# Optimization experiments

Measured on AMD Instinct MI355X. Metric: run time of the kernel, lower is better.

Reference implementation:

```python
import jax, jax.numpy as jnp
import numpy as np

VOCAB, S, D, H, DH, L, W1S, DFF = 50265, 4096, 768, 12, 64, 2, 256, 3072


def layer_norm(x, g, b, eps=1e-5):
    m = jnp.mean(x, axis=-1, keepdims=True)
    v = jnp.mean((x - m) ** 2, axis=-1, keepdims=True)
    return (x - m) * jax.lax.rsqrt(v + eps) * g + b


def sliding_global_attn(q, k, v, att, w=W1S):
    # q,k,v: [B,H,S,Dh]; att: [B,S] float (1 real / 0 pad). Longformer-style
    # sliding window (one-sided w) + global attention on token 0.
    B, nh, S_, Dh = q.shape
    nc = S_ // w
    q = q * (Dh ** -0.5)
    k_pad = jnp.pad(k, ((0, 0), (0, 0), (w, w), (0, 0)))
    v_pad = jnp.pad(v, ((0, 0), (0, 0), (w, w), (0, 0)))
    idx = jnp.arange(nc)[:, None] * w + jnp.arange(3 * w)[None, :]  # [nc,3w] into padded axis
    k_band = k_pad[:, :, idx]  # [B,H,nc,3w,Dh]
    v_band = v_pad[:, :, idx]
    qc = q.reshape(B, nh, nc, w, Dh)
    s_loc = jnp.einsum('bhcqd,bhckd->bhcqk', qc, k_band)  # [B,H,nc,w,3w]
    rel = jnp.arange(3 * w)[None, :] - jnp.arange(w)[:, None]  # [w,3w]
    band_ok = (rel >= 0) & (rel <= 2 * w)
    key_abs = idx - w  # [nc,3w] absolute key positions
    in_seq = (key_abs >= 0) & (key_abs < S_) & (key_abs != 0)  # token 0 handled by global column
    key_real = att[:, jnp.clip(key_abs, 0, S_ - 1)] > 0  # [B,nc,3w]
    valid = band_ok[None, None, None] & in_seq[None, None, :, None, :] & key_real[:, None, :, None, :]
    s_loc = jnp.where(valid, s_loc, -1e9)
    s_g = jnp.einsum('bhcqd,bhd->bhcq', qc, k[:, :, 0])  # global key column
    p = jax.nn.softmax(jnp.concatenate([s_g[..., None], s_loc], axis=-1), axis=-1)
    out = (jnp.einsum('bhcq,bhd->bhcqd', p[..., 0], v[:, :, 0])
           + jnp.einsum('bhcqk,bhckd->bhcqd', p[..., 1:], v_band)).reshape(B, nh, S_, Dh)
    # global token 0 attends to everything
    s0 = jnp.where(att[:, None, :] > 0, jnp.einsum('bhd,bhsd->bhs', q[:, :, 0], k), -1e9)
    out0 = jnp.einsum('bhs,bhsd->bhd', jax.nn.softmax(s0, axis=-1), v)
    return out.at[:, :, 0].set(out0)


def setup_inputs() -> dict:
    key = jax.random.key(0)
    ks = jax.random.split(key, 16)
    sc = 0.02
    inp = {
        'input_ids': jax.random.randint(ks[0], (2, S), 0, VOCAB, dtype=jnp.int64)
        if jax.config.jax_enable_x64 else jax.random.randint(ks[0], (2, S), 0, VOCAB, dtype=jnp.int32),
        'attention_mask': jnp.ones((2, S), dtype=jnp.int32),
        'word_emb': sc * jax.random.normal(ks[1], (VOCAB, D), jnp.float32),
        'pos_emb': sc * jax.random.normal(ks[2], (S, D), jnp.float32),
        'emb_ln_g': jnp.ones((D,), jnp.float32), 'emb_ln_b': jnp.zeros((D,), jnp.float32),
        'Wq': sc * jax.random.normal(ks[3], (L, D, D), jnp.float32), 'bq': jnp.zeros((L, D), jnp.float32),
        'Wk': sc * jax.random.normal(ks[4], (L, D, D), jnp.float32), 'bk': jnp.zeros((L, D), jnp.float32),
        'Wv': sc * jax.random.normal(ks[5], (L, D, D), jnp.float32), 'bv': jnp.zeros((L, D), jnp.float32),
        'Wo': sc * jax.random.normal(ks[6], (L, D, D), jnp.float32), 'bo': jnp.zeros((L, D), jnp.float32),
        'ln1_g': jnp.ones((L, D), jnp.float32), 'ln1_b': jnp.zeros((L, D), jnp.float32),
        'Wf1': sc * jax.random.normal(ks[7], (L, D, DFF), jnp.float32), 'bf1': jnp.zeros((L, DFF), jnp.float32),
        'Wf2': sc * jax.random.normal(ks[8], (L, DFF, D), jnp.float32), 'bf2': jnp.zeros((L, D), jnp.float32),
        'ln2_g': jnp.ones((L, D), jnp.float32), 'ln2_b': jnp.zeros((L, D), jnp.float32),
        'Wh1': sc * jax.random.normal(ks[9], (D, 256), jnp.float32), 'bh1': jnp.zeros((256,), jnp.float32),
        'Wh2': sc * jax.random.normal(ks[10], (256, 14), jnp.float32), 'bh2': jnp.zeros((14,), jnp.float32),
    }
    return inp


def reference(input_ids, attention_mask, word_emb, pos_emb, emb_ln_g, emb_ln_b,
              Wq, bq, Wk, bk, Wv, bv, Wo, bo, ln1_g, ln1_b,
              Wf1, bf1, Wf2, bf2, ln2_g, ln2_b, Wh1, bh1, Wh2, bh2):
    B, S_ = input_ids.shape
    att = attention_mask.astype(jnp.float32)
    x = word_emb[input_ids] + pos_emb[None, :S_, :]
    x = layer_norm(x, emb_ln_g, emb_ln_b)
    for l in range(L):
        def heads(w, b):
            return (x @ w + b).reshape(B, S_, H, DH).transpose(0, 2, 1, 3)
        q = heads(Wq[l], bq[l]); k = heads(Wk[l], bk[l]); v = heads(Wv[l], bv[l])
        a = sliding_global_attn(q, k, v, att)
        a = a.transpose(0, 2, 1, 3).reshape(B, S_, D) @ Wo[l] + bo[l]
        x = layer_norm(x + a, ln1_g[l], ln1_b[l])
        f = jax.nn.gelu(x @ Wf1[l] + bf1[l]) @ Wf2[l] + bf2[l]
        x = layer_norm(x + f, ln2_g[l], ln2_b[l])
    # masked mean pool
    m = att[..., None]
    pooled = jnp.sum(x * m, axis=1) / jnp.clip(jnp.sum(m, axis=1), 1e-9)
    h = jax.nn.relu(pooled @ Wh1 + bh1)
    return jax.nn.sigmoid(h @ Wh2 + bh2) * 4.0
```

## Files before the change

### kernel.cpp

```cpp
#include <hip/hip_runtime.h>
#include <hip/hip_bf16.h>
#include <math.h>

#define S_LEN 4096
#define D_MODEL 768
#define NHEAD 12
#define DH 64
#define NLAYER 2
#define DFF 3072
#define BATCH 2
#define QSTR 2304

typedef __attribute__((ext_vector_type(8))) __bf16 bf16x8;
typedef __attribute__((ext_vector_type(4))) float f32x4;
typedef __attribute__((ext_vector_type(16))) float f32x16;

__device__ __forceinline__ unsigned short f2bf_bits(float f) {
  unsigned int u = __float_as_uint(f);
  unsigned int r = (u + 0x7fffu + ((u >> 16) & 1u)) >> 16;
  return (unsigned short)r;
}

__device__ __forceinline__ float bf2f(unsigned short u) {
  return __uint_as_float(((unsigned int)u) << 16);
}

__device__ __forceinline__ unsigned int cvtpk_bf16(float lo, float hi) {
  unsigned int d;
  asm("v_cvt_pk_bf16_f32 %0, %1, %2" : "=v"(d) : "v"(lo), "v"(hi));
  return d;
}

__device__ __forceinline__ float gelu_fast(float x) {
  float u = 0.7978845608028654f * (x + 0.044715f * x * x * x);
  float t2 = fminf(fmaxf(2.f * u, -18.f), 18.f);
  float e = __expf(t2);
  return 0.5f * x * (1.f + (e - 1.f) / (e + 1.f));
}

#define ASYNC_COPY16(gsrc, ldst)                                       \
  __builtin_amdgcn_global_load_lds(                                    \
      (const __attribute__((address_space(1))) void*)(gsrc),           \
      (__attribute__((address_space(3))) void*)(ldst), 16, 0, 0)

#define MFMA_BF16(a, b, c) __builtin_amdgcn_mfma_f32_16x16x32_bf16(a, b, c, 0, 0, 0)
#define MFMA32_BF16(a, b, c) __builtin_amdgcn_mfma_f32_32x32x16_bf16(a, b, c, 0, 0, 0)

__device__ __forceinline__ float blk_sum256(float v, float* lds) {
#pragma unroll
  for (int off = 32; off > 0; off >>= 1) v += __shfl_down(v, off, 64);
  __syncthreads();
  if ((threadIdx.x & 63) == 0) lds[threadIdx.x >> 6] = v;
  __syncthreads();
  return lds[0] + lds[1] + lds[2] + lds[3];
}

__global__ __launch_bounds__(256) void wconv_kernel(
    const float* __restrict__ Wq, const float* __restrict__ Wk,
    const float* __restrict__ Wv, const float* __restrict__ Wo,
    const float* __restrict__ Wf1, const float* __restrict__ Wf2,
    unsigned short* __restrict__ Wbf) {
  int id = blockIdx.x;
  const float* src;
  unsigned short* dst;
  int K, N, t;
  if (id < 4608) {
    int m = id / 576;
    t = id % 576;
    int layer = m >> 2, which = m & 3;
    const float* s = (which == 0) ? Wq : (which == 1) ? Wk : (which == 2) ? Wv : Wo;
    src = s + (size_t)layer * 589824;
    dst = Wbf + (size_t)layer * 7077888 + (size_t)which * 589824;
    K = 768; N = 768;
  } else if (id < 9216) {
    int j = id - 4608;
    int layer = j / 2304;
    t = j % 2304;
    src = Wf1 + (size_t)layer * 2359296;
    dst = Wbf + (size_t)layer * 7077888 + 2359296;
    K = 768; N = 3072;
  } else {
    int j = id - 9216;
    int layer = j / 2304;
    t = j % 2304;
    src = Wf2 + (size_t)layer * 2359296;
    dst = Wbf + (size_t)layer * 7077888 + 4718592;
    K = 3072; N = 768;
  }
  int tiles_n = N >> 5;
  int tk = t / tiles_n, tn = t % tiles_n;
  __shared__ float tile[32][33];
  int c = threadIdx.x & 31, r0 = threadIdx.x >> 5;
#pragma unroll
  for (int p = 0; p < 4; ++p) {
    int r = r0 + p * 8;
    tile[r][c] = src[(size_t)(tk * 32 + r) * N + tn * 32 + c];
  }
  __syncthreads();
#pragma unroll
  for (int p = 0; p < 4; ++p) {
    int r = r0 + p * 8;
    dst[(size_t)(tn * 32 + r) * K + tk * 32 + c] = f2bf_bits(tile[c][r]);
  }
}

__global__ __launch_bounds__(256) void embed_ln_kernel(
    const int* __restrict__ ids, const float* __restrict__ wemb,
    const float* __restrict__ pemb, const float* __restrict__ g,
    const float* __restrict__ b, unsigned short* __restrict__ Xb) {
  int row = blockIdx.x;
  int s = row % S_LEN;
  int id = ids[row];
  const float* we = wemb + (size_t)id * D_MODEL;
  const float* pe = pemb + (size_t)s * D_MODEL;
  int t = threadIdx.x;
  __shared__ float lds[4];
  float v0 = we[t] + pe[t];
  float v1 = we[t + 256] + pe[t + 256];
  float v2 = we[t + 512] + pe[t + 512];
  float mean = blk_sum256(v0 + v1 + v2, lds) * (1.f / 768.f);
  float d0 = v0 - mean, d1 = v1 - mean, d2 = v2 - mean;
  float var = blk_sum256(d0 * d0 + d1 * d1 + d2 * d2, lds) * (1.f / 768.f);
  float rs = rsqrtf(var + 1e-5f);
  unsigned short* xb = Xb + (size_t)row * D_MODEL;
  xb[t]       = f2bf_bits(d0 * rs * g[t] + b[t]);
  xb[t + 256] = f2bf_bits(d1 * rs * g[t + 256] + b[t + 256]);
  xb[t + 512] = f2bf_bits(d2 * rs * g[t + 512] + b[t + 512]);
}

__global__ __launch_bounds__(256) void ln_kernel(
    const float* __restrict__ T, const float* __restrict__ g,
    const float* __restrict__ b, unsigned short* __restrict__ Xb) {
  int row = blockIdx.x;
  const float* tp = T + (size_t)row * D_MODEL;
  int t = threadIdx.x;
  __shared__ float lds[4];
  float v0 = tp[t], v1 = tp[t + 256], v2 = tp[t + 512];
  float mean = blk_sum256(v0 + v1 + v2, lds) * (1.f / 768.f);
  float d0 = v0 - mean, d1 = v1 - mean, d2 = v2 - mean;
  float var = blk_sum256(d0 * d0 + d1 * d1 + d2 * d2, lds) * (1.f / 768.f);
  float rs = rsqrtf(var + 1e-5f);
  unsigned short* xb = Xb + (size_t)row * D_MODEL;
  xb[t]       = f2bf_bits(d0 * rs * g[t] + b[t]);
  xb[t + 256] = f2bf_bits(d1 * rs * g[t + 256] + b[t + 256]);
  xb[t + 512] = f2bf_bits(d2 * rs * g[t + 512] + b[t + 512]);
}

template <int MODE>
__global__ __launch_bounds__(256) void gemm32(
    const unsigned short* __restrict__ A, const unsigned short* __restrict__ Bt,
    const float* __restrict__ bias0, const float* __restrict__ bias1,
    const float* __restrict__ bias2, const unsigned short* __restrict__ ResBf,
    void* __restrict__ Cout, int M, int N, int K) {
  __shared__ unsigned short Abuf[3][128 * 32];
  __shared__ unsigned short Bbuf[3][128 * 32];
  const int tid = threadIdx.x;
  const int lane = tid & 63, w = tid >> 6;
  const int wm = w >> 1, wn = w & 1;
  const int l31 = lane & 31, l5 = lane >> 5;

  const int nbx = gridDim.x;
  const int nwg = nbx * gridDim.y;
  const int orig = blockIdx.y * nbx + blockIdx.x;
  const int wgid = (orig & 7) * (nwg >> 3) + (orig >> 3);
  const int m0 = (wgid / nbx) * 128, n0 = (wgid % nbx) * 128;

  f32x16 acc[2][2];
#pragma unroll
  for (int i = 0; i < 2; ++i)
#pragma unroll
    for (int j = 0; j < 2; ++j)
#pragma unroll
      for (int r = 0; r < 16; ++r) acc[i][j][r] = 0.f;

  const int s0 = w * 64 + lane, s1 = s0 + 256;
  const int r0 = s0 >> 2, c0 = (s0 & 3) ^ ((r0 >> 1) & 3);
  const int r1 = s1 >> 2, c1 = (s1 & 3) ^ ((r1 >> 1) & 3);
  const unsigned short* gA0 = A + (size_t)(m0 + r0) * K + c0 * 8;
  const unsigned short* gA1 = A + (size_t)(m0 + r1) * K + c1 * 8;
  const unsigned short* gB0 = Bt + (size_t)(n0 + r0) * K + c0 * 8;
  const unsigned short* gB1 = Bt + (size_t)(n0 + r1) * K + c1 * 8;
  const int dA0 = (w * 64) * 8, dA1 = (256 + w * 64) * 8;

  int aoff[2][2], boff[2][2];
#pragma unroll
  for (int mt = 0; mt < 2; ++mt) {
    int ra = wm * 64 + mt * 32 + l31;
    int rb = wn * 64 + mt * 32 + l31;
    int key_a = (ra >> 1) & 3, key_b = (rb >> 1) & 3;
#pragma unroll
    for (int ks = 0; ks < 2; ++ks) {
      aoff[mt][ks] = ra * 32 + ((((ks << 1) | l5) ^ key_a) << 3);
      boff[mt][ks] = rb * 32 + ((((ks << 1) | l5) ^ key_b) << 3);
    }
  }

#define STAGE(bsel)                                                       \
  {                                                                       \
    ASYNC_COPY16(gA0, &Abuf[bsel][dA0]);                                  \
    ASYNC_COPY16(gA1, &Abuf[bsel][dA1]);                                  \
    ASYNC_COPY16(gB0, &Bbuf[bsel][dA0]);                                  \
    ASYNC_COPY16(gB1, &Bbuf[bsel][dA1]);                                  \
    gA0 += 32; gA1 += 32; gB0 += 32; gB1 += 32;                           \
  }

  const int nk = K >> 5;
  STAGE(0);
  if (nk > 1) STAGE(1);
  asm volatile("s_waitcnt vmcnt(4)" ::: "memory");
  __builtin_amdgcn_s_barrier();
  __builtin_amdgcn_sched_barrier(0);

  int cur = 0;
  for (int kt = 0; kt < nk; ++kt) {
    if (kt + 2 < nk) {
      int nxt = cur + 2;
      if (nxt >= 3) nxt -= 3;
      STAGE(nxt);
    }
    bf16x8 av[2][2], bv[2][2];
#pragma unroll
    for (int mt = 0; mt < 2; ++mt)
#pragma unroll
      for (int ks = 0; ks < 2; ++ks) {
        av[mt][ks] = *(const bf16x8*)(&Abuf[cur][aoff[mt][ks]]);
        bv[mt][ks] = *(const bf16x8*)(&Bbuf[cur][boff[mt][ks]]);
      }
#pragma unroll
    for (int mt = 0; mt < 2; ++mt)
#pragma unroll
      for (int nt = 0; nt < 2; ++nt)
#pragma unroll
        for (int ks = 0; ks < 2; ++ks)
          acc[mt][nt] = MFMA32_BF16(av[mt][ks], bv[nt][ks], acc[mt][nt]);
    if (kt + 1 < nk) {
      if (kt + 2 < nk)
        asm volatile("s_waitcnt vmcnt(4)" ::: "memory");
      else
        asm volatile("s_waitcnt vmcnt(0)" ::: "memory");
      __builtin_amdgcn_s_barrier();
      __builtin_amdgcn_sched_barrier(0);
    }
    cur = (cur == 2) ? 0 : cur + 1;
  }
#undef STAGE

#pragma unroll
  for (int mt = 0; mt < 2; ++mt) {
#pragma unroll
    for (int nt = 0; nt < 2; ++nt) {
      int gc = n0 + wn * 64 + nt * 32 + l31;
      float bsv;
      if (MODE == 4)
        bsv = (gc < 768) ? bias0[gc] : (gc < 1536) ? bias1[gc - 768] : bias2[gc - 1536];
      else
        bsv = bias0[gc];
#pragma unroll
      for (int reg = 0; reg < 16; ++reg) {
        int gr = m0 + wm * 64 + mt * 32 + (reg & 3) + 8 * (reg >> 2) + 4 * l5;
        float v = acc[mt][nt][reg] + bsv;
        if (MODE == 1) v = gelu_fast(v);
        if (MODE == 4 && gc < 768) v *= 0.125f;
        if (MODE == 2) {
          v += bf2f(ResBf[(size_t)gr * 768 + gc]);
          ((float*)Cout)[(size_t)gr * N + gc] = v;
        } else {
          ((unsigned short*)Cout)[(size_t)gr * N + gc] = f2bf_bits(v);
        }
      }
    }
  }
}

__global__ __launch_bounds__(256) void gemm_bf16_m1(
    const unsigned short* __restrict__ A, const unsigned short* __restrict__ Bt,
    const float* __restrict__ bias0, unsigned short* __restrict__ Cout,
    int M, int N, int K) {
  __shared__ unsigned short Abuf[3][128 * 32];
  __shared__ unsigned short Bbuf[3][128 * 32];
  const int tid = threadIdx.x;
  const int lane = tid & 63, w = tid >> 6;
  const int wm = w >> 1, wn = w & 1;

  const int nbx = gridDim.x;
  const int nwg = nbx * gridDim.y;
  const int orig = blockIdx.y * nbx + blockIdx.x;
  const int wgid = (orig & 7) * (nwg >> 3) + (orig >> 3);
  const int m0 = (wgid / nbx) * 128, n0 = (wgid % nbx) * 128;

  f32x4 acc[4][4];
#pragma unroll
  for (int i = 0; i < 4; ++i)
#pragma unroll
    for (int j = 0; j < 4; ++j) acc[i][j] = (f32x4){0.f, 0.f, 0.f, 0.f};

  const int s0 = w * 64 + lane, s1 = s0 + 256;
  const int r0 = s0 >> 2, c0 = (s0 & 3) ^ (r0 & 3);
  const int r1 = s1 >> 2, c1 = (s1 & 3) ^ (r1 & 3);
  const unsigned short* gA0 = A + (size_t)(m0 + r0) * K + c0 * 8;
  const unsigned short* gA1 = A + (size_t)(m0 + r1) * K + c1 * 8;
  const unsigned short* gB0 = Bt + (size_t)(n0 + r0) * K + c0 * 8;
  const unsigned short* gB1 = Bt + (size_t)(n0 + r1) * K + c1 * 8;
  const int dA0 = (w * 64) * 8, dA1 = (256 + w * 64) * 8;

  const int frow = lane & 15, kgrp = lane >> 4;
  int aoff[4], boff[4];
#pragma unroll
  for (int i = 0; i < 4; ++i) {
    int ra = wm * 64 + i * 16 + frow;
    int rb = wn * 64 + i * 16 + frow;
    aoff[i] = ra * 32 + ((kgrp ^ (ra & 3)) * 8);
    boff[i] = rb * 32 + ((kgrp ^ (rb & 3)) * 8);
  }

#define STAGE(bsel)                                                       \
  {                                                                       \
    ASYNC_COPY16(gA0, &Abuf[bsel][dA0]);                                  \
    ASYNC_COPY16(gA1, &Abuf[bsel][dA1]);                                  \
    ASYNC_COPY16(gB0, &Bbuf[bsel][dA0]);                                  \
    ASYNC_COPY16(gB1, &Bbuf[bsel][dA1]);                                  \
    gA0 += 32; gA1 += 32; gB0 += 32; gB1 += 32;                           \
  }

  const int nk = K >> 5;
  STAGE(0);
  if (nk > 1) STAGE(1);
  asm volatile("s_waitcnt vmcnt(4)" ::: "memory");
  __builtin_amdgcn_s_barrier();
  __builtin_amdgcn_sched_barrier(0);

  int cur = 0;
  for (int kt = 0; kt < nk; ++kt) {
    if (kt + 2 < nk) {
      int nxt = cur + 2;
      if (nxt >= 3) nxt -= 3;
      STAGE(nxt);
    }
    bf16x8 av[4], bv[4];
#pragma unroll
    for (int i = 0; i < 4; ++i) av[i] = *(const bf16x8*)(&Abuf[cur][aoff[i]]);
#pragma unroll
    for (int j = 0; j < 4; ++j) bv[j] = *(const bf16x8*)(&Bbuf[cur][boff[j]]);
#pragma unroll
    for (int i = 0; i < 4; ++i)
#pragma unroll
      for (int j = 0; j < 4; ++j)
        acc[i][j] = MFMA_BF16(av[i], bv[j], acc[i][j]);
    if (kt + 1 < nk) {
      if (kt + 2 < nk)
        asm volatile("s_waitcnt vmcnt(4)" ::: "memory");
      else
        asm volatile("s_waitcnt vmcnt(0)" ::: "memory");
      __builtin_amdgcn_s_barrier();
      __builtin_amdgcn_sched_barrier(0);
    }
    cur = (cur == 2) ? 0 : cur + 1;
  }
#undef STAGE

#pragma unroll
  for (int i = 0; i < 4; ++i) {
#pragma unroll
    for (int j = 0; j < 4; ++j) {
      int grb = m0 + wm * 64 + i * 16 + (lane >> 4) * 4;
      int gc = n0 + wn * 64 + j * 16 + (lane & 15);
      float bsv = bias0[gc];
#pragma unroll
      for (int r = 0; r < 4; ++r) {
        float v = gelu_fast(acc[i][j][r] + bsv);
        Cout[(size_t)(grb + r) * N + gc] = f2bf_bits(v);
      }
    }
  }
}

__global__ __launch_bounds__(256) void vtrans_kernel(
    const unsigned short* __restrict__ Vsrc, unsigned short* __restrict__ Vt) {
  int kb = blockIdx.x, h = blockIdx.y, b = blockIdx.z;
  int k0 = kb * 64;
  const size_t bs = (size_t)b * S_LEN;
  const size_t bh = (size_t)(b * NHEAD + h);
  __shared__ unsigned short tile[64][72];
  int tid = threadIdx.x;
#pragma unroll
  for (int p = 0; p < 2; ++p) {
    int idx = p * 256 + tid;
    int key = idx >> 3, ch = idx & 7;
    bf16x8 v = *(const bf16x8*)(Vsrc + (bs + k0 + key) * QSTR + h * DH + ch * 8);
    *(bf16x8*)&tile[key][ch * 8] = v;
  }
  __syncthreads();
#pragma unroll
  for (int p = 0; p < 2; ++p) {
    int idx = p * 256 + tid;
    int d = idx >> 3, kc = idx & 7;
    unsigned int w0 = tile[kc * 8 + 0][d] | ((unsigned int)tile[kc * 8 + 1][d] << 16);
    unsigned int w1 = tile[kc * 8 + 2][d] | ((unsigned int)tile[kc * 8 + 3][d] << 16);
    unsigned int w2 = tile[kc * 8 + 4][d] | ((unsigned int)tile[kc * 8 + 5][d] << 16);
    unsigned int w3 = tile[kc * 8 + 6][d] | ((unsigned int)tile[kc * 8 + 7][d] << 16);
    uint4 out = make_uint4(w0, w1, w2, w3);
    *(uint4*)(Vt + (bh * 64 + d) * S_LEN + k0 + kc * 8) = out;
  }
}

__global__ __launch_bounds__(512) void band_attn_kernel(
    const unsigned short* __restrict__ Qg, const unsigned short* __restrict__ Kgb,
    const unsigned short* __restrict__ Vgb, const unsigned short* __restrict__ Vt,
    const int* __restrict__ att, unsigned short* __restrict__ Aout) {
  const int c = blockIdx.x, h = blockIdx.y, b = blockIdx.z;
  const int tid = threadIdx.x;
  const int lane = tid & 63, wq = tid >> 6;
  const int g = lane >> 4, cl = lane & 15;
  const size_t bs = (size_t)b * S_LEN;
  const size_t bh = (size_t)(b * NHEAD + h);

  __shared__ __align__(16) char smem[18944];

  if (c == 16) {
    float* sc = (float*)smem;
    float* q0 = sc + S_LEN;
    float* red = q0 + 64;
    float* part = red + 8;
    if (tid < 64) q0[tid] = bf2f(Qg[bs * QSTR + h * DH + tid]);
    __syncthreads();
    float lmax = -1e30f;
    for (int s = tid; s < S_LEN; s += 512) {
      const unsigned short* kp = Kgb + (bs + s) * QSTR + h * DH;
      float acc = 0.f;
#pragma unroll
      for (int cc = 0; cc < 8; ++cc) {
        uint4 u = *(const uint4*)(kp + cc * 8);
        const unsigned int* uu = (const unsigned int*)&u;
#pragma unroll
        for (int w2 = 0; w2 < 4; ++w2) {
          unsigned int x = uu[w2];
          acc += q0[cc * 8 + w2 * 2] * __uint_as_float(x << 16);
          acc += q0[cc * 8 + w2 * 2 + 1] * __uint_as_float(x & 0xffff0000u);
        }
      }
      acc = (att[b * S_LEN + s] > 0) ? acc : -1e9f;
      sc[s] = acc;
      lmax = fmaxf(lmax, acc);
    }
#pragma unroll
    for (int off = 32; off > 0; off >>= 1) lmax = fmaxf(lmax, __shfl_down(lmax, off, 64));
    __syncthreads();
    if (lane == 0) red[wq] = lmax;
    __syncthreads();
    float M = red[0];
#pragma unroll
    for (int i = 1; i < 8; ++i) M = fmaxf(M, red[i]);
    float lsum = 0.f;
    for (int s = tid; s < S_LEN; s += 512) {
      float p = __expf(sc[s] - M);
      sc[s] = p;
      lsum += p;
    }
#pragma unroll
    for (int off = 32; off > 0; off >>= 1) lsum += __shfl_down(lsum, off, 64);
    __syncthreads();
    if (lane == 0) red[wq] = lsum;
    __syncthreads();
    float L = red[0];
#pragma unroll
    for (int i = 1; i < 8; ++i) L += red[i];
    int d = tid & 63, chunk = tid >> 6;
    float acc2 = 0.f;
    for (int s = chunk * 512; s < (chunk + 1) * 512; ++s)
      acc2 += sc[s] * bf2f(Vgb[(bs + s) * QSTR + h * DH + d]);
    part[chunk * 64 + d] = acc2;
    __syncthreads();
    if (tid < 64) {
      float v = 0.f;
#pragma unroll
      for (int i = 0; i < 8; ++i) v += part[i * 64 + tid];
      Aout[bs * D_MODEL + h * DH + tid] = f2bf_bits(v / L);
    }
    return;
  }

  unsigned short* Klds = (unsigned short*)smem;
  unsigned short* Vlds = Klds + 64 * 64;
  float* kmask = (float*)(Vlds + 64 * 64);

  bf16x8 qf[2][2];
#pragma unroll
  for (int qt = 0; qt < 2; ++qt)
#pragma unroll
    for (int ks = 0; ks < 2; ++ks)
      qf[qt][ks] = *(const bf16x8*)(Qg + (bs + c * 256 + wq * 32 + qt * 16 + cl) * QSTR +
                                    h * DH + ks * 32 + g * 8);

  float mrun[2], lrun[2];
  f32x4 oacc[2][4];
#pragma unroll
  for (int qt = 0; qt < 2; ++qt) {
    float sg = 0.f;
#pragma unroll
    for (int ks = 0; ks < 2; ++ks) {
      bf16x8 k0 = *(const bf16x8*)(Kgb + bs * QSTR + h * DH + ks * 32 + g * 8);
#pragma unroll
      for (int j = 0; j < 8; ++j) sg += (float)qf[qt][ks][j] * (float)k0[j];
    }
    sg += __shfl_xor(sg, 16, 64);
    sg += __shfl_xor(sg, 32, 64);
    mrun[qt] = sg;
    lrun[qt] = 1.f;
  }
#pragma unroll
  for (int dt = 0; dt < 4; ++dt) {
    float v0d = bf2f(Vgb[bs * QSTR + h * DH + dt * 16 + cl]);
    f32x4 vv = {v0d, v0d, v0d, v0d};
    oacc[0][dt] = vv;
    oacc[1][dt] = vv;
  }

  const int jlo = wq * 32, jhi = wq * 32 + 543;

  for (int t = 0; t < 12; ++t) {
    int kabs0 = c * 256 - 256 + t * 64;
    if (kabs0 < 0 || kabs0 >= S_LEN) continue;
    __syncthreads();
    {
      int key = tid >> 3, ch = tid & 7;
      bf16x8 kv = *(const bf16x8*)(Kgb + (bs + kabs0 + key) * QSTR + h * DH + ch * 8);
      *(bf16x8*)(Klds + key * 64 + ((ch ^ (key & 7)) * 8)) = kv;
      bf16x8 vv = *(const bf16x8*)(Vt + (bh * 64 + key) * S_LEN + kabs0 + ch * 8);
      *(bf16x8*)(Vlds + key * 64 + ((ch ^ (key & 7)) * 8)) = vv;
      if (tid < 64) {
        int ka = kabs0 + tid;
        kmask[tid] = (ka >= 1 && att[b * S_LEN + ka] > 0) ? 0.f : -1e9f;
      }
    }
    __syncthreads();
    if (t * 64 + 63 < jlo || t * 64 > jhi) continue;

    f32x4 accs[4][2];
#pragma unroll
    for (int kt = 0; kt < 4; ++kt) {
      accs[kt][0] = (f32x4){0.f, 0.f, 0.f, 0.f};
      accs[kt][1] = (f32x4){0.f, 0.f, 0.f, 0.f};
    }
#pragma unroll
    for (int ks = 0; ks < 2; ++ks) {
      bf16x8 kf[4];
#pragma unroll
      for (int kt = 0; kt < 4; ++kt) {
        int key = kt * 16 + cl;
        kf[kt] = *(const bf16x8*)(Klds + key * 64 + (((ks * 4 + g) ^ (key & 7)) * 8));
      }
#pragma unroll
      for (int kt = 0; kt < 4; ++kt) {
        accs[kt][0] = MFMA_BF16(kf[kt], qf[0][ks], accs[kt][0]);
        accs[kt][1] = MFMA_BF16(kf[kt], qf[1][ks], accs[kt][1]);
      }
    }

#pragma unroll
    for (int qt = 0; qt < 2; ++qt) {
      int iq = wq * 32 + qt * 16 + cl;
      int relbase = t * 64 - iq;
      float pvv[4][4];
      float tmax = -1e30f;
#pragma unroll
      for (int kt = 0; kt < 4; ++kt)
#pragma unroll
        for (int r = 0; r < 4; ++r) {
          int key = kt * 16 + g * 4 + r;
          int rel = relbase + key;
          float x = accs[kt][qt][r] + kmask[key];
          x = (rel >= 0 && rel <= 512) ? x : -1e9f;
          pvv[kt][r] = x;
          tmax = fmaxf(tmax, x);
        }
      tmax = fmaxf(tmax, __shfl_xor(tmax, 16, 64));
      tmax = fmaxf(tmax, __shfl_xor(tmax, 32, 64));
      float mnew = fmaxf(mrun[qt], tmax);
      float scale = __expf(mrun[qt] - mnew);
      mrun[qt] = mnew;
      float psum = 0.f;
#pragma unroll
      for (int kt = 0; kt < 4; ++kt)
#pragma unroll
        for (int r = 0; r < 4; ++r) {
          float p = __expf(pvv[kt][r] - mnew);
          pvv[kt][r] = p;
          psum += p;
        }
      psum += __shfl_xor(psum, 16, 64);
      psum += __shfl_xor(psum, 32, 64);
      lrun[qt] = lrun[qt] * scale + psum;
      float scr[4];
#pragma unroll
      for (int r = 0; r < 4; ++r) scr[r] = __shfl(scale, g * 4 + r, 64);
#pragma unroll
      for (int dt = 0; dt < 4; ++dt) {
        oacc[qt][dt][0] *= scr[0];
        oacc[qt][dt][1] *= scr[1];
        oacc[qt][dt][2] *= scr[2];
        oacc[qt][dt][3] *= scr[3];
      }
#pragma unroll
      for (int ks = 0; ks < 2; ++ks) {
        unsigned int E0D0 = cvtpk_bf16(pvv[ks * 2][0], pvv[ks * 2][1]);
        unsigned int E0D1 = cvtpk_bf16(pvv[ks * 2][2], pvv[ks * 2][3]);
        unsigned int E1D0 = cvtpk_bf16(pvv[ks * 2 + 1][0], pvv[ks * 2 + 1][1]);
        unsigned int E1D1 = cvtpk_bf16(pvv[ks * 2 + 1][2], pvv[ks * 2 + 1][3]);
        int src0 = ((lane >> 4) & 1) * 32 + cl;
        int src1 = src0 + 16;
        unsigned int a0 = (unsigned int)__shfl((int)E0D0, src0, 64);
        unsigned int a1 = (unsigned int)__shfl((int)E0D1, src0, 64);
        unsigned int a2 = (unsigned int)__shfl((int)E0D0, src1, 64);
        unsigned int a3 = (unsigned int)__shfl((int)E0D1, src1, 64);
        unsigned int b0 = (unsigned int)__shfl((int)E1D0, src0, 64);
        unsigned int b1 = (unsigned int)__shfl((int)E1D1, src0, 64);
        unsigned int b2 = (unsigned int)__shfl((int)E1D0, src1, 64);
        unsigned int b3 = (unsigned int)__shfl((int)E1D1, src1, 64);
        bool hi = lane >= 32;
        union { unsigned int u[4]; bf16x8 v; } af;
        af.u[0] = hi ? b0 : a0;
        af.u[1] = hi ? b1 : a1;
        af.u[2] = hi ? b2 : a2;
        af.u[3] = hi ? b3 : a3;
#pragma unroll
        for (int dt = 0; dt < 4; ++dt) {
          int d = dt * 16 + cl;
          bf16x8 vf = *(const bf16x8*)(Vlds + d * 64 + (((ks * 4 + g) ^ (d & 7)) * 8));
          oacc[qt][dt] = MFMA_BF16(af.v, vf, oacc[qt][dt]);
        }
      }
    }
  }

#pragma unroll
  for (int qt = 0; qt < 2; ++qt) {
    float lr[4];
#pragma unroll
    for (int r = 0; r < 4; ++r) lr[r] = 1.f / __shfl(lrun[qt], g * 4 + r, 64);
#pragma unroll
    for (int dt = 0; dt < 4; ++dt)
#pragma unroll
      for (int r = 0; r < 4; ++r) {
        int row = c * 256 + wq * 32 + qt * 16 + g * 4 + r;
        if (row != 0)
          Aout[(bs + row) * D_MODEL + h * DH + dt * 16 + cl] =
              f2bf_bits(oacc[qt][dt][r] * lr[r]);
      }
  }
}

__global__ __launch_bounds__(256) void pool1_kernel(
    const unsigned short* __restrict__ Xb, const int* __restrict__ att,
    float* __restrict__ ppart) {
  int sb = blockIdx.x, b = blockIdx.y, t = threadIdx.x;
  float a0 = 0.f, a1 = 0.f, a2 = 0.f;
  for (int s = sb * 256; s < sb * 256 + 256; ++s) {
    float a = (float)att[b * S_LEN + s];
    const unsigned short* xp = Xb + ((size_t)b * S_LEN + s) * D_MODEL;
    a0 += bf2f(xp[t]) * a; a1 += bf2f(xp[t + 256]) * a; a2 += bf2f(xp[t + 512]) * a;
  }
  float* pp = ppart + ((size_t)b * 16 + sb) * D_MODEL;
  pp[t] = a0; pp[t + 256] = a1; pp[t + 512] = a2;
}

__global__ __launch_bounds__(256) void pool2_kernel(
    const float* __restrict__ ppart, const int* __restrict__ att,
    float* __restrict__ pooled) {
  int b = blockIdx.x, t = threadIdx.x;
  float a0 = 0.f, a1 = 0.f, a2 = 0.f;
  for (int sb = 0; sb < 16; ++sb) {
    const float* pp = ppart + ((size_t)b * 16 + sb) * D_MODEL;
    a0 += pp[t]; a1 += pp[t + 256]; a2 += pp[t + 512];
  }
  float cnt = 0.f;
  for (int s = 0; s < S_LEN; ++s) cnt += (float)att[b * S_LEN + s];
  cnt = fmaxf(cnt, 1e-9f);
  pooled[b * D_MODEL + t]       = a0 / cnt;
  pooled[b * D_MODEL + t + 256] = a1 / cnt;
  pooled[b * D_MODEL + t + 512] = a2 / cnt;
}

__global__ __launch_bounds__(256) void head_kernel(
    const float* __restrict__ pooled, const float* __restrict__ Wh1,
    const float* __restrict__ bh1, const float* __restrict__ Wh2,
    const float* __restrict__ bh2, float* __restrict__ out) {
  __shared__ float hbuf[2][256];
  int t = threadIdx.x;
  for (int b = 0; b < 2; ++b) {
    float acc = bh1[t];
    for (int d = 0; d < D_MODEL; ++d) acc += pooled[b * D_MODEL + d] * Wh1[d * 256 + t];
    hbuf[b][t] = fmaxf(acc, 0.f);
  }
  __syncthreads();
  if (t < 28) {
    int b = t / 14, j = t % 14;
    float acc = bh2[j];
    for (int i = 0; i < 256; ++i) acc += hbuf[b][i] * Wh2[i * 14 + j];
    out[t] = 4.f / (1.f + __expf(-acc));
  }
}

extern "C" void kernel_launch(void* const* d_in, const int* in_sizes, int n_in,
                              void* d_out, int out_size, void* d_ws,
                              size_t ws_size, hipStream_t stream) {
  const int* ids    = (const int*)d_in[0];
  const int* att    = (const int*)d_in[1];
  const float* wemb = (const float*)d_in[2];
  const float* pemb = (const float*)d_in[3];
  const float* elng = (const float*)d_in[4];
  const float* elnb = (const float*)d_in[5];
  const float* Wq   = (const float*)d_in[6];
  const float* bq   = (const float*)d_in[7];
  const float* Wk   = (const float*)d_in[8];
  const float* bk   = (const float*)d_in[9];
  const float* Wv   = (const float*)d_in[10];
  const float* bv   = (const float*)d_in[11];
  const float* Wo   = (const float*)d_in[12];
  const float* bo   = (const float*)d_in[13];
  const float* ln1g = (const float*)d_in[14];
  const float* ln1b = (const float*)d_in[15];
  const float* Wf1  = (const float*)d_in[16];
  const float* bf1  = (const float*)d_in[17];
  const float* Wf2  = (const float*)d_in[18];
  const float* bf2  = (const float*)d_in[19];
  const float* ln2g = (const float*)d_in[20];
  const float* ln2b = (const float*)d_in[21];
  const float* Wh1  = (const float*)d_in[22];
  const float* bh1  = (const float*)d_in[23];
  const float* Wh2  = (const float*)d_in[24];
  const float* bh2  = (const float*)d_in[25];

  const int M = BATCH * S_LEN;
  float* ws = (float*)d_ws;
  float* T = ws;
  unsigned short* QKV  = (unsigned short*)(ws + 6291456);
  unsigned short* Vt   = (unsigned short*)(ws + 11010048);
  unsigned short* Abbf = (unsigned short*)(ws + 12582912);
  unsigned short* Xbf  = (unsigned short*)(ws + 15728640);
  unsigned short* FFbf = (unsigned short*)(ws + 18874368);
  unsigned short* Wbf  = (unsigned short*)(ws + 31457280);
  float* pooled = ws + 38535168;
  float* ppart  = ws + 38536704;

  wconv_kernel<<<13824, 256, 0, stream>>>(Wq, Wk, Wv, Wo, Wf1, Wf2, Wbf);
  embed_ln_kernel<<<M, 256, 0, stream>>>(ids, wemb, pemb, elng, elnb, Xbf);

  for (int l = 0; l < NLAYER; ++l) {
    const unsigned short* wqkv = Wbf + (size_t)l * 7077888;
    const unsigned short* wot  = wqkv + 1769472;
    const unsigned short* wf1t = wqkv + 2359296;
    const unsigned short* wf2t = wqkv + 4718592;

    gemm32<4><<<dim3(18, 64), 256, 0, stream>>>(
        Xbf, wqkv, bq + l * D_MODEL, bk + l * D_MODEL, bv + l * D_MODEL,
        nullptr, QKV, M, QSTR, 768);

    vtrans_kernel<<<dim3(64, NHEAD, BATCH), 256, 0, stream>>>(QKV + 1536, Vt);
    band_attn_kernel<<<dim3(17, NHEAD, BATCH), 512, 0, stream>>>(
        QKV, QKV + 768, QKV + 1536, Vt, att, Abbf);

    gemm32<2><<<dim3(6, 64), 256, 0, stream>>>(
        Abbf, wot, bo + l * D_MODEL, nullptr, nullptr, Xbf, T, M, 768, 768);
    ln_kernel<<<M, 256, 0, stream>>>(T, ln1g + l * D_MODEL, ln1b + l * D_MODEL, Xbf);

    if (l == 0)
      gemm_bf16_m1<<<dim3(24, 64), 256, 0, stream>>>(
          Xbf, wf1t, bf1 + l * DFF, FFbf, M, DFF, 768);
    else
      gemm32<1><<<dim3(24, 64), 256, 0, stream>>>(
          Xbf, wf1t, bf1 + l * DFF, nullptr, nullptr, nullptr, FFbf, M, DFF, 768);

    gemm32<2><<<dim3(6, 64), 256, 0, stream>>>(
        FFbf, wf2t, bf2 + l * D_MODEL, nullptr, nullptr, Xbf, T, M, 768, DFF);
    ln_kernel<<<M, 256, 0, stream>>>(T, ln2g + l * D_MODEL, ln2b + l * D_MODEL, Xbf);
  }

  pool1_kernel<<<dim3(16, BATCH), 256, 0, stream>>>(Xbf, att, ppart);
  pool2_kernel<<<BATCH, 256, 0, stream>>>(ppart, att, pooled);
  head_kernel<<<1, 256, 0, stream>>>(pooled, Wh1, bh1, Wh2, bh2, (float*)d_out);
}
```

Baseline: 830.8 us.

## Double-buffer K/V tiles in band attention and halve query block size

Restructures the band attention kernel so each block handles 128 queries (one 16-row tile per wave) instead of 256, doubling the grid to 33 blocks per head. K/V tiles are double-buffered in LDS, with the next tile's global loads issued before computing the current one, and the tile range is clipped to the valid band rather than skipped in the loop. It also drops the specialized first-layer FFN1 GEMM and uses the generic gemm32<1> for both layers. The intent is more parallelism and overlap of loads with MFMA work, at the cost of re-reading more overlapping K/V per query and using more LDS per block.

Measured after the change: 998.3 us. +20.2%, slower.

```diff
diff --git a/kernel.cpp b/kernel.cpp
--- a/kernel.cpp
+++ b/kernel.cpp
@@ -272,108 +272,6 @@
   }
 }
 
-__global__ __launch_bounds__(256) void gemm_bf16_m1(
-    const unsigned short* __restrict__ A, const unsigned short* __restrict__ Bt,
-    const float* __restrict__ bias0, unsigned short* __restrict__ Cout,
-    int M, int N, int K) {
-  __shared__ unsigned short Abuf[3][128 * 32];
-  __shared__ unsigned short Bbuf[3][128 * 32];
-  const int tid = threadIdx.x;
-  const int lane = tid & 63, w = tid >> 6;
-  const int wm = w >> 1, wn = w & 1;
-
-  const int nbx = gridDim.x;
-  const int nwg = nbx * gridDim.y;
-  const int orig = blockIdx.y * nbx + blockIdx.x;
-  const int wgid = (orig & 7) * (nwg >> 3) + (orig >> 3);
-  const int m0 = (wgid / nbx) * 128, n0 = (wgid % nbx) * 128;
-
-  f32x4 acc[4][4];
-#pragma unroll
-  for (int i = 0; i < 4; ++i)
-#pragma unroll
-    for (int j = 0; j < 4; ++j) acc[i][j] = (f32x4){0.f, 0.f, 0.f, 0.f};
-
-  const int s0 = w * 64 + lane, s1 = s0 + 256;
-  const int r0 = s0 >> 2, c0 = (s0 & 3) ^ (r0 & 3);
-  const int r1 = s1 >> 2, c1 = (s1 & 3) ^ (r1 & 3);
-  const unsigned short* gA0 = A + (size_t)(m0 + r0) * K + c0 * 8;
-  const unsigned short* gA1 = A + (size_t)(m0 + r1) * K + c1 * 8;
-  const unsigned short* gB0 = Bt + (size_t)(n0 + r0) * K + c0 * 8;
-  const unsigned short* gB1 = Bt + (size_t)(n0 + r1) * K + c1 * 8;
-  const int dA0 = (w * 64) * 8, dA1 = (256 + w * 64) * 8;
-
-  const int frow = lane & 15, kgrp = lane >> 4;
-  int aoff[4], boff[4];
-#pragma unroll
-  for (int i = 0; i < 4; ++i) {
-    int ra = wm * 64 + i * 16 + frow;
-    int rb = wn * 64 + i * 16 + frow;
-    aoff[i] = ra * 32 + ((kgrp ^ (ra & 3)) * 8);
-    boff[i] = rb * 32 + ((kgrp ^ (rb & 3)) * 8);
-  }
-
-#define STAGE(bsel)                                                       \
-  {                                                                       \
-    ASYNC_COPY16(gA0, &Abuf[bsel][dA0]);                                  \
-    ASYNC_COPY16(gA1, &Abuf[bsel][dA1]);                                  \
-    ASYNC_COPY16(gB0, &Bbuf[bsel][dA0]);                                  \
-    ASYNC_COPY16(gB1, &Bbuf[bsel][dA1]);                                  \
-    gA0 += 32; gA1 += 32; gB0 += 32; gB1 += 32;                           \
-  }
-
-  const int nk = K >> 5;
-  STAGE(0);
-  if (nk > 1) STAGE(1);
-  asm volatile("s_waitcnt vmcnt(4)" ::: "memory");
-  __builtin_amdgcn_s_barrier();
-  __builtin_amdgcn_sched_barrier(0);
-
-  int cur = 0;
-  for (int kt = 0; kt < nk; ++kt) {
-    if (kt + 2 < nk) {
-      int nxt = cur + 2;
-      if (nxt >= 3) nxt -= 3;
-      STAGE(nxt);
-    }
-    bf16x8 av[4], bv[4];
-#pragma unroll
-    for (int i = 0; i < 4; ++i) av[i] = *(const bf16x8*)(&Abuf[cur][aoff[i]]);
-#pragma unroll
-    for (int j = 0; j < 4; ++j) bv[j] = *(const bf16x8*)(&Bbuf[cur][boff[j]]);
-#pragma unroll
-    for (int i = 0; i < 4; ++i)
-#pragma unroll
-      for (int j = 0; j < 4; ++j)
-        acc[i][j] = MFMA_BF16(av[i], bv[j], acc[i][j]);
-    if (kt + 1 < nk) {
-      if (kt + 2 < nk)
-        asm volatile("s_waitcnt vmcnt(4)" ::: "memory");
-      else
-        asm volatile("s_waitcnt vmcnt(0)" ::: "memory");
-      __builtin_amdgcn_s_barrier();
-      __builtin_amdgcn_sched_barrier(0);
-    }
-    cur = (cur == 2) ? 0 : cur + 1;
-  }
-#undef STAGE
-
-#pragma unroll
-  for (int i = 0; i < 4; ++i) {
-#pragma unroll
-    for (int j = 0; j < 4; ++j) {
-      int grb = m0 + wm * 64 + i * 16 + (lane >> 4) * 4;
-      int gc = n0 + wn * 64 + j * 16 + (lane & 15);
-      float bsv = bias0[gc];
-#pragma unroll
-      for (int r = 0; r < 4; ++r) {
-        float v = gelu_fast(acc[i][j][r] + bsv);
-        Cout[(size_t)(grb + r) * N + gc] = f2bf_bits(v);
-      }
-    }
-  }
-}
-
 __global__ __launch_bounds__(256) void vtrans_kernel(
     const unsigned short* __restrict__ Vsrc, unsigned short* __restrict__ Vt) {
   int kb = blockIdx.x, h = blockIdx.y, b = blockIdx.z;
@@ -414,9 +312,9 @@
   const size_t bs = (size_t)b * S_LEN;
   const size_t bh = (size_t)(b * NHEAD + h);
 
-  __shared__ __align__(16) char smem[18944];
-
-  if (c == 16) {
+  __shared__ __align__(16) char smem[33280];
+
+  if (c == 32) {
     float* sc = (float*)smem;
     float* q0 = sc + S_LEN;
     float* red = q0 + 64;
@@ -480,173 +378,185 @@
   }
 
   unsigned short* Klds = (unsigned short*)smem;
-  unsigned short* Vlds = Klds + 64 * 64;
-  float* kmask = (float*)(Vlds + 64 * 64);
-
-  bf16x8 qf[2][2];
-#pragma unroll
-  for (int qt = 0; qt < 2; ++qt)
-#pragma unroll
-    for (int ks = 0; ks < 2; ++ks)
-      qf[qt][ks] = *(const bf16x8*)(Qg + (bs + c * 256 + wq * 32 + qt * 16 + cl) * QSTR +
-                                    h * DH + ks * 32 + g * 8);
-
-  float mrun[2], lrun[2];
-  f32x4 oacc[2][4];
-#pragma unroll
-  for (int qt = 0; qt < 2; ++qt) {
+  unsigned short* Vlds = Klds + 2 * 4096;
+  float* kmask = (float*)(Vlds + 2 * 4096);
+
+  const int Q0 = c * 128;
+
+  bf16x8 qf[2];
+#pragma unroll
+  for (int ks = 0; ks < 2; ++ks)
+    qf[ks] = *(const bf16x8*)(Qg + (bs + Q0 + wq * 16 + cl) * QSTR +
+                              h * DH + ks * 32 + g * 8);
+
+  float mrun, lrun;
+  f32x4 oacc[4];
+  {
     float sg = 0.f;
 #pragma unroll
     for (int ks = 0; ks < 2; ++ks) {
       bf16x8 k0 = *(const bf16x8*)(Kgb + bs * QSTR + h * DH + ks * 32 + g * 8);
 #pragma unroll
-      for (int j = 0; j < 8; ++j) sg += (float)qf[qt][ks][j] * (float)k0[j];
+      for (int j = 0; j < 8; ++j) sg += (float)qf[ks][j] * (float)k0[j];
     }
     sg += __shfl_xor(sg, 16, 64);
     sg += __shfl_xor(sg, 32, 64);
-    mrun[qt] = sg;
-    lrun[qt] = 1.f;
-  }
-#pragma unroll
-  for (int dt = 0; dt < 4; ++dt) {
-    float v0d = bf2f(Vgb[bs * QSTR + h * DH + dt * 16 + cl]);
-    f32x4 vv = {v0d, v0d, v0d, v0d};
-    oacc[0][dt] = vv;
-    oacc[1][dt] = vv;
-  }
-
-  const int jlo = wq * 32, jhi = wq * 32 + 543;
-
-  for (int t = 0; t < 12; ++t) {
-    int kabs0 = c * 256 - 256 + t * 64;
-    if (kabs0 < 0 || kabs0 >= S_LEN) continue;
-    __syncthreads();
-    {
-      int key = tid >> 3, ch = tid & 7;
-      bf16x8 kv = *(const bf16x8*)(Kgb + (bs + kabs0 + key) * QSTR + h * DH + ch * 8);
-      *(bf16x8*)(Klds + key * 64 + ((ch ^ (key & 7)) * 8)) = kv;
-      bf16x8 vv = *(const bf16x8*)(Vt + (bh * 64 + key) * S_LEN + kabs0 + ch * 8);
-      *(bf16x8*)(Vlds + key * 64 + ((ch ^ (key & 7)) * 8)) = vv;
-      if (tid < 64) {
-        int ka = kabs0 + tid;
-        kmask[tid] = (ka >= 1 && att[b * S_LEN + ka] > 0) ? 0.f : -1e9f;
-      }
-    }
-    __syncthreads();
-    if (t * 64 + 63 < jlo || t * 64 > jhi) continue;
-
-    f32x4 accs[4][2];
-#pragma unroll
-    for (int kt = 0; kt < 4; ++kt) {
-      accs[kt][0] = (f32x4){0.f, 0.f, 0.f, 0.f};
-      accs[kt][1] = (f32x4){0.f, 0.f, 0.f, 0.f};
-    }
+    mrun = sg;
+    lrun = 1.f;
+#pragma unroll
+    for (int dt = 0; dt < 4; ++dt) {
+      float v0d = bf2f(Vgb[bs * QSTR + h * DH + dt * 16 + cl]);
+      oacc[dt] = (f32x4){v0d, v0d, v0d, v0d};
+    }
+  }
+
+  const int jwlo = wq * 16, jwhi = wq * 16 + 543;
+  const int tlo = (Q0 < 256) ? ((256 - Q0) >> 6) : 0;
+  int thi = (S_LEN - Q0 + 256) >> 6;
+  if (thi > 10) thi = 10;
+
+  const int skey = tid >> 3, sch = tid & 7;
+  const int swz = (sch ^ (skey & 7)) * 8;
+
+  auto LOADT = [&](int t, bf16x8& kr, bf16x8& vr) {
+    int kb0 = Q0 - 256 + t * 64;
+    kr = *(const bf16x8*)(Kgb + (bs + kb0 + skey) * QSTR + h * DH + sch * 8);
+    vr = *(const bf16x8*)(Vt + (bh * 64 + skey) * S_LEN + kb0 + sch * 8);
+  };
+  auto WRITET = [&](int p, int t, bf16x8 kr, bf16x8 vr) {
+    *(bf16x8*)(Klds + p * 4096 + skey * 64 + swz) = kr;
+    *(bf16x8*)(Vlds + p * 4096 + skey * 64 + swz) = vr;
+    if (tid < 64) {
+      int ka = Q0 - 256 + t * 64 + tid;
+      kmask[p * 64 + tid] = (ka >= 1 && att[b * S_LEN + ka] > 0) ? 0.f : -1e9f;
+    }
+  };
+
+  auto COMPUTE = [&](int p, int t) {
+    if (t * 64 + 63 < jwlo || t * 64 > jwhi) return;
+    f32x4 accs[4];
+#pragma unroll
+    for (int kt = 0; kt < 4; ++kt) accs[kt] = (f32x4){0.f, 0.f, 0.f, 0.f};
 #pragma unroll
     for (int ks = 0; ks < 2; ++ks) {
       bf16x8 kf[4];
 #pragma unroll
       for (int kt = 0; kt < 4; ++kt) {
         int key = kt * 16 + cl;
-        kf[kt] = *(const bf16x8*)(Klds + key * 64 + (((ks * 4 + g) ^ (key & 7)) * 8));
+        kf[kt] = *(const bf16x8*)(Klds + p * 4096 + key * 64 +
+                                  (((ks * 4 + g) ^ (key & 7)) * 8));
       }
 #pragma unroll
-      for (int kt = 0; kt < 4; ++kt) {
-        accs[kt][0] = MFMA_BF16(kf[kt], qf[0][ks], accs[kt][0]);
-        accs[kt][1] = MFMA_BF16(kf[kt], qf[1][ks], accs[kt][1]);
+      for (int kt = 0; kt < 4; ++kt)
+        accs[kt] = MFMA_BF16(kf[kt], qf[ks], accs[kt]);
+    }
+
+    int iq = wq * 16 + cl;
+    int relbase = t * 64 - iq;
+    float pvv[4][4];
+    float tmax = -1e30f;
+#pragma unroll
+    for (int kt = 0; kt < 4; ++kt)
+#pragma unroll
+      for (int r = 0; r < 4; ++r) {
+        int key = kt * 16 + g * 4 + r;
+        int rel = relbase + key;
+        float x = accs[kt][r] + kmask[p * 64 + key];
+        x = (rel >= 0 && rel <= 512) ? x : -1e9f;
+        pvv[kt][r] = x;
+        tmax = fmaxf(tmax, x);
       }
-    }
-
-#pragma unroll
-    for (int qt = 0; qt < 2; ++qt) {
-      int iq = wq * 32 + qt * 16 + cl;
-      int relbase = t * 64 - iq;
-      float pvv[4][4];
-      float tmax = -1e30f;
-#pragma unroll
-      for (int kt = 0; kt < 4; ++kt)
-#pragma unroll
-        for (int r = 0; r < 4; ++r) {
-          int key = kt * 16 + g * 4 + r;
-          int rel = relbase + key;
-          float x = accs[kt][qt][r] + kmask[key];
-          x = (rel >= 0 && rel <= 512) ? x : -1e9f;
-          pvv[kt][r] = x;
-          tmax = fmaxf(tmax, x);
-        }
-      tmax = fmaxf(tmax, __shfl_xor(tmax, 16, 64));
-      tmax = fmaxf(tmax, __shfl_xor(tmax, 32, 64));
-      float mnew = fmaxf(mrun[qt], tmax);
-      float scale = __expf(mrun[qt] - mnew);
-      mrun[qt] = mnew;
-      float psum = 0.f;
-#pragma unroll
-      for (int kt = 0; kt < 4; ++kt)
-#pragma unroll
-        for (int r = 0; r < 4; ++r) {
-          float p = __expf(pvv[kt][r] - mnew);
-          pvv[kt][r] = p;
-          psum += p;
-        }
-      psum += __shfl_xor(psum, 16, 64);
-      psum += __shfl_xor(psum, 32, 64);
-      lrun[qt] = lrun[qt] * scale + psum;
-      float scr[4];
-#pragma unroll
-      for (int r = 0; r < 4; ++r) scr[r] = __shfl(scale, g * 4 + r, 64);
+    tmax = fmaxf(tmax, __shfl_xor(tmax, 16, 64));
+    tmax = fmaxf(tmax, __shfl_xor(tmax, 32, 64));
+    float mnew = fmaxf(mrun, tmax);
+    float scale = __expf(mrun - mnew);
+    mrun = mnew;
+    float psum = 0.f;
+#pragma unroll
+    for (int kt = 0; kt < 4; ++kt)
+#pragma unroll
+      for (int r = 0; r < 4; ++r) {
+        float pp = __expf(pvv[kt][r] - mnew);
+        pvv[kt][r] = pp;
+        psum += pp;
+      }
+    psum += __shfl_xor(psum, 16, 64);
+    psum += __shfl_xor(psum, 32, 64);
+    lrun = lrun * scale + psum;
+    float scr[4];
+#pragma unroll
+    for (int r = 0; r < 4; ++r) scr[r] = __shfl(scale, g * 4 + r, 64);
+#pragma unroll
+    for (int dt = 0; dt < 4; ++dt) {
+      oacc[dt][0] *= scr[0];
+      oacc[dt][1] *= scr[1];
+      oacc[dt][2] *= scr[2];
+      oacc[dt][3] *= scr[3];
+    }
+#pragma unroll
+    for (int ks = 0; ks < 2; ++ks) {
+      unsigned int E0D0 = cvtpk_bf16(pvv[ks * 2][0], pvv[ks * 2][1]);
+      unsigned int E0D1 = cvtpk_bf16(pvv[ks * 2][2], pvv[ks * 2][3]);
+      unsigned int E1D0 = cvtpk_bf16(pvv[ks * 2 + 1][0], pvv[ks * 2 + 1][1]);
+      unsigned int E1D1 = cvtpk_bf16(pvv[ks * 2 + 1][2], pvv[ks * 2 + 1][3]);
+      int src0 = ((lane >> 4) & 1) * 32 + cl;
+      int src1 = src0 + 16;
+      unsigned int a0 = (unsigned int)__shfl((int)E0D0, src0, 64);
+      unsigned int a1 = (unsigned int)__shfl((int)E0D1, src0, 64);
+      unsigned int a2 = (unsigned int)__shfl((int)E0D0, src1, 64);
+      unsigned int a3 = (unsigned int)__shfl((int)E0D1, src1, 64);
+      unsigned int b0 = (unsigned int)__shfl((int)E1D0, src0, 64);
+      unsigned int b1 = (unsigned int)__shfl((int)E1D1, src0, 64);
+      unsigned int b2 = (unsigned int)__shfl((int)E1D0, src1, 64);
+      unsigned int b3 = (unsigned int)__shfl((int)E1D1, src1, 64);
+      bool hi = lane >= 32;
+      union { unsigned int u[4]; bf16x8 v; } af;
+      af.u[0] = hi ? b0 : a0;
+      af.u[1] = hi ? b1 : a1;
+      af.u[2] = hi ? b2 : a2;
+      af.u[3] = hi ? b3 : a3;
 #pragma unroll
       for (int dt = 0; dt < 4; ++dt) {
-        oacc[qt][dt][0] *= scr[0];
-        oacc[qt][dt][1] *= scr[1];
-        oacc[qt][dt][2] *= scr[2];
-        oacc[qt][dt][3] *= scr[3];
+        int d = dt * 16 + cl;
+        bf16x8 vf = *(const bf16x8*)(Vlds + p * 4096 + d * 64 +
+                                     (((ks * 4 + g) ^ (d & 7)) * 8));
+        oacc[dt] = MFMA_BF16(af.v, vf, oacc[dt]);
       }
-#pragma unroll
-      for (int ks = 0; ks < 2; ++ks) {
-        unsigned int E0D0 = cvtpk_bf16(pvv[ks * 2][0], pvv[ks * 2][1]);
-        unsigned int E0D1 = cvtpk_bf16(pvv[ks * 2][2], pvv[ks * 2][3]);
-        unsigned int E1D0 = cvtpk_bf16(pvv[ks * 2 + 1][0], pvv[ks * 2 + 1][1]);
-        unsigned int E1D1 = cvtpk_bf16(pvv[ks * 2 + 1][2], pvv[ks * 2 + 1][3]);
-        int src0 = ((lane >> 4) & 1) * 32 + cl;
-        int src1 = src0 + 16;
-        unsigned int a0 = (unsigned int)__shfl((int)E0D0, src0, 64);
-        unsigned int a1 = (unsigned int)__shfl((int)E0D1, src0, 64);
-        unsigned int a2 = (unsigned int)__shfl((int)E0D0, src1, 64);
-        unsigned int a3 = (unsigned int)__shfl((int)E0D1, src1, 64);
-        unsigned int b0 = (unsigned int)__shfl((int)E1D0, src0, 64);
-        unsigned int b1 = (unsigned int)__shfl((int)E1D1, src0, 64);
-        unsigned int b2 = (unsigned int)__shfl((int)E1D0, src1, 64);
-        unsigned int b3 = (unsigned int)__shfl((int)E1D1, src1, 64);
-        bool hi = lane >= 32;
-        union { unsigned int u[4]; bf16x8 v; } af;
-        af.u[0] = hi ? b0 : a0;
-        af.u[1] = hi ? b1 : a1;
-        af.u[2] = hi ? b2 : a2;
-        af.u[3] = hi ? b3 : a3;
-#pragma unroll
-        for (int dt = 0; dt < 4; ++dt) {
-          int d = dt * 16 + cl;
-          bf16x8 vf = *(const bf16x8*)(Vlds + d * 64 + (((ks * 4 + g) ^ (d & 7)) * 8));
-          oacc[qt][dt] = MFMA_BF16(af.v, vf, oacc[qt][dt]);
-        }
-      }
-    }
-  }
-
-#pragma unroll
-  for (int qt = 0; qt < 2; ++qt) {
-    float lr[4];
-#pragma unroll
-    for (int r = 0; r < 4; ++r) lr[r] = 1.f / __shfl(lrun[qt], g * 4 + r, 64);
-#pragma unroll
-    for (int dt = 0; dt < 4; ++dt)
-#pragma unroll
-      for (int r = 0; r < 4; ++r) {
-        int row = c * 256 + wq * 32 + qt * 16 + g * 4 + r;
-        if (row != 0)
-          Aout[(bs + row) * D_MODEL + h * DH + dt * 16 + cl] =
-              f2bf_bits(oacc[qt][dt][r] * lr[r]);
-      }
-  }
+    }
+  };
+
+  bf16x8 kA, vA, kB, vB;
+  LOADT(tlo, kA, vA);
+  for (int t = tlo; t < thi; t += 2) {
+    __builtin_amdgcn_s_barrier();
+    WRITET(0, t, kA, vA);
+    if (t + 1 < thi) LOADT(t + 1, kB, vB);
+    asm volatile("s_waitcnt lgkmcnt(0)" ::: "memory");
+    __builtin_amdgcn_s_barrier();
+    __builtin_amdgcn_sched_barrier(0);
+    COMPUTE(0, t);
+    if (t + 1 >= thi) break;
+    __builtin_amdgcn_s_barrier();
+    WRITET(1, t + 1, kB, vB);
+    if (t + 2 < thi) LOADT(t + 2, kA, vA);
+    asm volatile("s_waitcnt lgkmcnt(0)" ::: "memory");
+    __builtin_amdgcn_s_barrier();
+    __builtin_amdgcn_sched_barrier(0);
+    COMPUTE(1, t + 1);
+  }
+
+  float lr[4];
+#pragma unroll
+  for (int r = 0; r < 4; ++r) lr[r] = 1.f / __shfl(lrun, g * 4 + r, 64);
+#pragma unroll
+  for (int dt = 0; dt < 4; ++dt)
+#pragma unroll
+    for (int r = 0; r < 4; ++r) {
+      int row = Q0 + wq * 16 + g * 4 + r;
+      if (row != 0)
+        Aout[(bs + row) * D_MODEL + h * DH + dt * 16 + cl] =
+            f2bf_bits(oacc[dt][r] * lr[r]);
+    }
 }
 
 __global__ __launch_bounds__(256) void pool1_kernel(
@@ -756,20 +666,15 @@
         nullptr, QKV, M, QSTR, 768);
 
     vtrans_kernel<<<dim3(64, NHEAD, BATCH), 256, 0, stream>>>(QKV + 1536, Vt);
-    band_attn_kernel<<<dim3(17, NHEAD, BATCH), 512, 0, stream>>>(
+    band_attn_kernel<<<dim3(33, NHEAD, BATCH), 512, 0, stream>>>(
         QKV, QKV + 768, QKV + 1536, Vt, att, Abbf);
 
     gemm32<2><<<dim3(6, 64), 256, 0, stream>>>(
         Abbf, wot, bo + l * D_MODEL, nullptr, nullptr, Xbf, T, M, 768, 768);
     ln_kernel<<<M, 256, 0, stream>>>(T, ln1g + l * D_MODEL, ln1b + l * D_MODEL, Xbf);
 
-    if (l == 0)
-      gemm_bf16_m1<<<dim3(24, 64), 256, 0, stream>>>(
-          Xbf, wf1t, bf1 + l * DFF, FFbf, M, DFF, 768);
-    else
-      gemm32<1><<<dim3(24, 64), 256, 0, stream>>>(
-          Xbf, wf1t, bf1 + l * DFF, nullptr, nullptr, nullptr, FFbf, M, DFF, 768);
-
+    gemm32<1><<<dim3(24, 64), 256, 0, stream>>>(
+        Xbf, wf1t, bf1 + l * DFF, nullptr, nullptr, nullptr, FFbf, M, DFF, 768);
     gemm32<2><<<dim3(6, 64), 256, 0, stream>>>(
         FFbf, wf2t, bf2 + l * D_MODEL, nullptr, nullptr, Xbf, T, M, 768, DFF);
     ln_kernel<<<M, 256, 0, stream>>>(T, ln2g + l * D_MODEL, ln2b + l * D_MODEL, Xbf);
```
